# Kernel tuning notes

Measured on AMD Instinct MI355X. Metric: run time of the kernel, lower is better.

## Reference

```python
import jax, jax.numpy as jnp
import numpy as np

B, T, D = 8, 2048, 64        # d_tok = 64
V = 4096                     # active codebook size (current_size = init_vocab)
GUMBEL_TAU = 0.7             # self.gumbel_tau
EPS = 1e-12                  # F.normalize eps


def _l2norm(v):
    return v / jnp.maximum(jnp.linalg.norm(v, axis=-1, keepdims=True), EPS)


def setup_inputs() -> dict:
    key = jax.random.key(0)
    k1, k2, k3 = jax.random.split(key, 3)
    x = jax.random.normal(k1, (B, T, D), dtype=jnp.float32)
    # codebook = nn.Embedding(max_vocab, d_tok) with std = d_tok**-0.5; only first V rows are active
    codebook = jax.random.normal(k2, (V, D), dtype=jnp.float32) * (D ** -0.5)
    # pre-sampled standard Gumbel noise for F.gumbel_softmax (deterministic reference)
    gumbel_noise = jax.random.gumbel(k3, (B * T, V), dtype=jnp.float32)
    return {"x": x, "codebook": codebook, "gumbel_noise": gumbel_noise}


def reference(x, codebook, gumbel_noise):
    b, t, d = x.shape
    x_flat = x.reshape(-1, d)                      # (N, D)
    x_norm = _l2norm(x_flat)
    cb_norm = _l2norm(codebook)                    # (V, D)
    sims = x_norm @ cb_norm.T                      # (N, V) cosine similarity
    indices = jnp.argmax(sims, axis=-1)            # (N,) nearest code
    # F.gumbel_softmax(sims, tau, hard=False): softmax((logits + g) / tau)
    soft = jax.nn.softmax((sims + gumbel_noise) / GUMBEL_TAU, axis=-1)
    # assign_st = one_hot + soft - sg(soft); assign_st @ codebook without materializing one_hot:
    #   primal  = codebook[indices]
    #   grad-to-codebook = one_hot^T @ g (scatter via the gather's VJP)
    #   grad-to-soft     = g @ sg(codebook)^T  (codebook treated as primal constant there)
    term = soft @ jax.lax.stop_gradient(codebook)  # (N, D)
    z_q_flat = codebook[indices] + term - jax.lax.stop_gradient(term)
    z_q = z_q_flat.reshape(b, t, d)
    # double straight-through: z_q_ste = x + sg(z_q - x) + (z_q - sg(z_q))
    z_q_ste = x + jax.lax.stop_gradient(z_q - x) + (z_q - jax.lax.stop_gradient(z_q))
    return z_q_ste, indices.reshape(b, t)
```

## Files before the change

kernel.cpp:

```cpp
#include <hip/hip_runtime.h>


constexpr int N_ROWS = 16384;
constexpr int D      = 64;
constexpr int V      = 4096;
constexpr int BM     = 64;
constexpr int BV     = 128;
constexpr int LS     = 68;
constexpr int NT     = V / BV;

__global__ void normalize_cb(const float* __restrict__ cb, float* __restrict__ cbn) {
    int row = blockIdx.x * blockDim.x + threadIdx.x;
    if (row >= V) return;
    const float4* src = reinterpret_cast<const float4*>(cb + row * D);
    float4 v[16];
    float ss = 0.f;
#pragma unroll
    for (int i = 0; i < 16; ++i) {
        v[i] = src[i];
        ss += v[i].x * v[i].x + v[i].y * v[i].y + v[i].z * v[i].z + v[i].w * v[i].w;
    }
    float inv = 1.0f / fmaxf(sqrtf(ss), 1e-12f);
    float4* dst = reinterpret_cast<float4*>(cbn + row * D);
#pragma unroll
    for (int i = 0; i < 16; ++i)
        dst[i] = make_float4(v[i].x * inv, v[i].y * inv, v[i].z * inv, v[i].w * inv);
}

__global__ __launch_bounds__(256) void quantize(const float* __restrict__ x,
                                                const float* __restrict__ cb,
                                                const float* __restrict__ cbn,
                                                float* __restrict__ out) {
    __shared__ float xs[BM * LS];
    __shared__ float bs[BV * LS];
    const int tid = threadIdx.x;
    const int tc = tid & 15;
    const int tr = tid >> 4;
    const int row0 = blockIdx.x * BM;

#pragma unroll
    for (int p = 0; p < 4; ++p) {
        int flat = p * 1024 + tid * 4;
        int r = flat >> 6, k = flat & 63;
        float4 v = *reinterpret_cast<const float4*>(x + row0 * D + flat);
        *reinterpret_cast<float4*>(&xs[r * LS + k]) = v;
    }

    float best_v[4];
    int   best_i[4];
#pragma unroll
    for (int m = 0; m < 4; ++m) { best_v[m] = -1e30f; best_i[m] = 0; }

    for (int t = 0; t < NT; ++t) {
        __syncthreads();
#pragma unroll
        for (int p = 0; p < 8; ++p) {
            int flat = p * 1024 + tid * 4;
            int r = flat >> 6, k = flat & 63;
            float4 v = *reinterpret_cast<const float4*>(cbn + t * BV * D + flat);
            *reinterpret_cast<float4*>(&bs[r * LS + k]) = v;
        }
        __syncthreads();

        float acc[4][8];
#pragma unroll
        for (int m = 0; m < 4; ++m)
#pragma unroll
            for (int n = 0; n < 8; ++n) acc[m][n] = 0.f;

#pragma unroll
        for (int kk = 0; kk < D; kk += 4) {
            float4 a[4], b[8];
#pragma unroll
            for (int m = 0; m < 4; ++m)
                a[m] = *reinterpret_cast<const float4*>(&xs[(tr + 16 * m) * LS + kk]);
#pragma unroll
            for (int n = 0; n < 8; ++n)
                b[n] = *reinterpret_cast<const float4*>(&bs[(tc + 16 * n) * LS + kk]);
#pragma unroll
            for (int m = 0; m < 4; ++m)
#pragma unroll
                for (int n = 0; n < 8; ++n) {
                    acc[m][n] = fmaf(a[m].x, b[n].x, acc[m][n]);
                    acc[m][n] = fmaf(a[m].y, b[n].y, acc[m][n]);
                    acc[m][n] = fmaf(a[m].z, b[n].z, acc[m][n]);
                    acc[m][n] = fmaf(a[m].w, b[n].w, acc[m][n]);
                }
        }

#pragma unroll
        for (int m = 0; m < 4; ++m)
#pragma unroll
            for (int n = 0; n < 8; ++n) {
                int code = t * BV + tc + 16 * n;
                if (acc[m][n] > best_v[m]) { best_v[m] = acc[m][n]; best_i[m] = code; }
            }
    }

    __syncthreads();
    float* rv = bs;
    int*   ri = reinterpret_cast<int*>(bs + BM * 17);
#pragma unroll
    for (int m = 0; m < 4; ++m) {
        int row = tr + 16 * m;
        rv[row * 17 + tc] = best_v[m];
        ri[row * 17 + tc] = best_i[m];
    }
    int* fin = reinterpret_cast<int*>(xs);
    __syncthreads();
    if (tid < BM) {
        float bv = rv[tid * 17];
        int   bi = ri[tid * 17];
#pragma unroll
        for (int c = 1; c < 16; ++c) {
            float v = rv[tid * 17 + c];
            int   i = ri[tid * 17 + c];
            if (v > bv || (v == bv && i < bi)) { bv = v; bi = i; }
        }
        fin[tid] = bi;
        out[N_ROWS * D + row0 + tid] = (float)bi;
    }
    __syncthreads();

    {
        int row = tid >> 2, part = tid & 3;
        const float4* src = reinterpret_cast<const float4*>(cb + fin[row] * D) + part * 4;
        float4*       dst = reinterpret_cast<float4*>(out + (row0 + row) * D) + part * 4;
#pragma unroll
        for (int i = 0; i < 4; ++i) dst[i] = src[i];
    }
}

extern "C" void kernel_launch(void* const* d_in, const int* in_sizes, int n_in,
                              void* d_out, int out_size, void* d_ws, size_t ws_size,
                              hipStream_t stream) {
    const float* x   = (const float*)d_in[0];
    const float* cb  = (const float*)d_in[1];
    float* cbn = (float*)d_ws;
    float* out = (float*)d_out;

    normalize_cb<<<V / 256, 256, 0, stream>>>(cb, cbn);
    quantize<<<N_ROWS / BM, 256, 0, stream>>>(x, cb, cbn, out);
}
```

Measured before the change: 479.2 us.

## Split codebook search across blocks and merge partial argmax in separate kernel

The quantize kernel now splits the codebook into four chunks, so each block scans a quarter of the codes. This quadruples the grid from 256 to 1024 blocks and improves occupancy across the GPU's compute units. Per-chunk best values and indices go to workspace, and a new merge_gather kernel reduces them and gathers the codebook rows into the output. The codebook normalization is also parallelised to 16 threads per row with shuffle reductions. The cost is an extra kernel launch plus a round trip of partial results through global memory.

```diff
diff --git a/kernel.cpp b/kernel.cpp
--- a/kernel.cpp
+++ b/kernel.cpp
@@ -5,45 +5,47 @@
 constexpr int D      = 64;
 constexpr int V      = 4096;
 constexpr int BM     = 64;
-constexpr int BV     = 128;
+constexpr int BN     = 128;
+constexpr int NCH    = 4;
+constexpr int VCHUNK = V / NCH;
+constexpr int NT     = VCHUNK / BN;
 constexpr int LS     = 68;
-constexpr int NT     = V / BV;
 
-__global__ void normalize_cb(const float* __restrict__ cb, float* __restrict__ cbn) {
-    int row = blockIdx.x * blockDim.x + threadIdx.x;
-    if (row >= V) return;
-    const float4* src = reinterpret_cast<const float4*>(cb + row * D);
-    float4 v[16];
-    float ss = 0.f;
-#pragma unroll
-    for (int i = 0; i < 16; ++i) {
-        v[i] = src[i];
-        ss += v[i].x * v[i].x + v[i].y * v[i].y + v[i].z * v[i].z + v[i].w * v[i].w;
-    }
+__global__ __launch_bounds__(256) void normalize_cb(const float* __restrict__ cb,
+                                                    float* __restrict__ cbn) {
+    int g = blockIdx.x * 256 + threadIdx.x;
+    int row = g >> 4, part = g & 15;
+    float4 v = *reinterpret_cast<const float4*>(cb + row * D + part * 4);
+    float ss = v.x * v.x + v.y * v.y + v.z * v.z + v.w * v.w;
+    ss += __shfl_xor(ss, 1);
+    ss += __shfl_xor(ss, 2);
+    ss += __shfl_xor(ss, 4);
+    ss += __shfl_xor(ss, 8);
     float inv = 1.0f / fmaxf(sqrtf(ss), 1e-12f);
-    float4* dst = reinterpret_cast<float4*>(cbn + row * D);
-#pragma unroll
-    for (int i = 0; i < 16; ++i)
-        dst[i] = make_float4(v[i].x * inv, v[i].y * inv, v[i].z * inv, v[i].w * inv);
+    *reinterpret_cast<float4*>(cbn + row * D + part * 4) =
+        make_float4(v.x * inv, v.y * inv, v.z * inv, v.w * inv);
 }
 
-__global__ __launch_bounds__(256) void quantize(const float* __restrict__ x,
-                                                const float* __restrict__ cb,
-                                                const float* __restrict__ cbn,
-                                                float* __restrict__ out) {
+__global__ __launch_bounds__(256, 3) void quantize(const float* __restrict__ x,
+                                                   const float* __restrict__ cbn,
+                                                   float* __restrict__ pv,
+                                                   int* __restrict__ pi) {
     __shared__ float xs[BM * LS];
-    __shared__ float bs[BV * LS];
+    __shared__ float bs[BN * LS];
     const int tid = threadIdx.x;
     const int tc = tid & 15;
     const int tr = tid >> 4;
-    const int row0 = blockIdx.x * BM;
+    const int rowblk = blockIdx.x & (N_ROWS / BM - 1);
+    const int chunk  = blockIdx.x >> 8;
+    const int row0  = rowblk * BM;
+    const int vbase = chunk * VCHUNK;
 
 #pragma unroll
     for (int p = 0; p < 4; ++p) {
-        int flat = p * 1024 + tid * 4;
-        int r = flat >> 6, k = flat & 63;
-        float4 v = *reinterpret_cast<const float4*>(x + row0 * D + flat);
-        *reinterpret_cast<float4*>(&xs[r * LS + k]) = v;
+        int f = p * 256 + tid;
+        int r = f >> 4, k4 = f & 15;
+        float4 v = *reinterpret_cast<const float4*>(x + row0 * D + f * 4);
+        *reinterpret_cast<float4*>(&xs[r * LS + k4 * 4]) = v;
     }
 
     float best_v[4];
@@ -55,10 +57,10 @@
         __syncthreads();
 #pragma unroll
         for (int p = 0; p < 8; ++p) {
-            int flat = p * 1024 + tid * 4;
-            int r = flat >> 6, k = flat & 63;
-            float4 v = *reinterpret_cast<const float4*>(cbn + t * BV * D + flat);
-            *reinterpret_cast<float4*>(&bs[r * LS + k]) = v;
+            int f = p * 256 + tid;
+            int r = f >> 4, k4 = f & 15;
+            float4 v = *reinterpret_cast<const float4*>(cbn + (vbase + t * BN) * D + f * 4);
+            *reinterpret_cast<float4*>(&bs[r * LS + k4 * 4]) = v;
         }
         __syncthreads();
 
@@ -92,21 +94,20 @@
         for (int m = 0; m < 4; ++m)
 #pragma unroll
             for (int n = 0; n < 8; ++n) {
-                int code = t * BV + tc + 16 * n;
+                int code = vbase + t * BN + tc + 16 * n;
                 if (acc[m][n] > best_v[m]) { best_v[m] = acc[m][n]; best_i[m] = code; }
             }
     }
 
     __syncthreads();
-    float* rv = bs;
-    int*   ri = reinterpret_cast<int*>(bs + BM * 17);
+    float* rv = xs;
+    int*   ri = reinterpret_cast<int*>(xs + BM * 17);
 #pragma unroll
     for (int m = 0; m < 4; ++m) {
         int row = tr + 16 * m;
         rv[row * 17 + tc] = best_v[m];
         ri[row * 17 + tc] = best_i[m];
     }
-    int* fin = reinterpret_cast<int*>(xs);
     __syncthreads();
     if (tid < BM) {
         float bv = rv[tid * 17];
@@ -117,28 +118,44 @@
             int   i = ri[tid * 17 + c];
             if (v > bv || (v == bv && i < bi)) { bv = v; bi = i; }
         }
-        fin[tid] = bi;
-        out[N_ROWS * D + row0 + tid] = (float)bi;
+        pv[chunk * N_ROWS + row0 + tid] = bv;
+        pi[chunk * N_ROWS + row0 + tid] = bi;
     }
-    __syncthreads();
+}
 
-    {
-        int row = tid >> 2, part = tid & 3;
-        const float4* src = reinterpret_cast<const float4*>(cb + fin[row] * D) + part * 4;
-        float4*       dst = reinterpret_cast<float4*>(out + (row0 + row) * D) + part * 4;
+__global__ __launch_bounds__(256) void merge_gather(const float* __restrict__ pv,
+                                                    const int* __restrict__ pi,
+                                                    const float* __restrict__ cb,
+                                                    float* __restrict__ out) {
+    int g = blockIdx.x * 256 + threadIdx.x;
+    int row = g >> 2, q = g & 3;
+    float bv = pv[row];
+    int   bi = pi[row];
 #pragma unroll
-        for (int i = 0; i < 4; ++i) dst[i] = src[i];
+    for (int c = 1; c < NCH; ++c) {
+        float v = pv[c * N_ROWS + row];
+        int   i = pi[c * N_ROWS + row];
+        if (v > bv) { bv = v; bi = i; }
     }
+    if (q == 0) out[N_ROWS * D + row] = (float)bi;
+    const float4* src = reinterpret_cast<const float4*>(cb + bi * D) + q * 4;
+    float4*       dst = reinterpret_cast<float4*>(out + row * D) + q * 4;
+#pragma unroll
+    for (int i = 0; i < 4; ++i) dst[i] = src[i];
 }
 
 extern "C" void kernel_launch(void* const* d_in, const int* in_sizes, int n_in,
                               void* d_out, int out_size, void* d_ws, size_t ws_size,
                               hipStream_t stream) {
-    const float* x   = (const float*)d_in[0];
-    const float* cb  = (const float*)d_in[1];
+    const float* x  = (const float*)d_in[0];
+    const float* cb = (const float*)d_in[1];
     float* cbn = (float*)d_ws;
+    float* pv  = (float*)((char*)d_ws + (size_t)V * D * 4);
+    int*   pi  = (int*)  ((char*)d_ws + (size_t)V * D * 4
+                                      + (size_t)NCH * N_ROWS * 4);
     float* out = (float*)d_out;
 
-    normalize_cb<<<V / 256, 256, 0, stream>>>(cb, cbn);
-    quantize<<<N_ROWS / BM, 256, 0, stream>>>(x, cb, cbn, out);
+    normalize_cb<<<V * 16 / 256, 256, 0, stream>>>(cb, cbn);
+    quantize<<<(N_ROWS / BM) * NCH, 256, 0, stream>>>(x, cbn, pv, pi);
+    merge_gather<<<N_ROWS * 4 / 256, 256, 0, stream>>>(pv, pi, cb, out);
 }
```

Result: faster. 429.8 us (-10.3%).
